# Kernel tuning notes

Measured on AMD Instinct MI355X. Metric: run time of the kernel, lower is better.

The kernel has to match this reference:

```python
import jax, jax.numpy as jnp
import numpy as np

EMBED = 1024
HEADS = 16
HEAD_DIM = EMBED // HEADS


def setup_inputs() -> dict:
    key = jax.random.key(0)
    ks = jax.random.split(key, 8)
    N, L = 2, 2048
    s = 0.02
    return {
        "values": jax.random.normal(ks[0], (N, L, EMBED), jnp.float32),
        "keys": jax.random.normal(ks[1], (N, L, EMBED), jnp.float32),
        "queries": jax.random.normal(ks[2], (N, L, EMBED), jnp.float32),
        # per-head projection weights, SHARED across heads (nn.Linear(head_dim, head_dim))
        "Wv": jax.random.normal(ks[3], (HEAD_DIM, HEAD_DIM), jnp.float32) * s,
        "Wk": jax.random.normal(ks[4], (HEAD_DIM, HEAD_DIM), jnp.float32) * s,
        "Wq": jax.random.normal(ks[5], (HEAD_DIM, HEAD_DIM), jnp.float32) * s,
        "Wo": jax.random.normal(ks[6], (EMBED, EMBED), jnp.float32) * s,
        "bo": jax.random.normal(ks[7], (EMBED,), jnp.float32) * s,
    }


def reference(values, keys, queries, Wv, Wk, Wq, Wo, bo):
    N, Lq, _ = queries.shape
    Lk = keys.shape[1]
    Lv = values.shape[1]
    # split heads: (N, L, H, D)
    v = values.reshape(N, Lv, HEADS, HEAD_DIM)
    k = keys.reshape(N, Lk, HEADS, HEAD_DIM)
    q = queries.reshape(N, Lq, HEADS, HEAD_DIM)
    # per-head linear (weight shared across heads); nn.Linear computes x @ W.T
    v = jnp.einsum('nlhd,ed->nlhe', v, Wv)
    k = jnp.einsum('nlhd,ed->nlhe', k, Wk)
    q = jnp.einsum('nlhd,ed->nlhe', q, Wq)
    # scores (N, H, Lq, Lk); NOTE: scale uses sqrt(embed_size), as in the original
    scores = jnp.einsum('nqhd,nkhd->nhqk', q, k) / jnp.sqrt(jnp.float32(EMBED))
    attn = jax.nn.softmax(scores, axis=-1)
    out = jnp.einsum('nhql,nlhd->nqhd', attn, v).reshape(N, Lq, EMBED)
    out = out @ Wo.T + bo
    return out
```

## Files before the change

### kernel.cpp

```cpp
#include <hip/hip_runtime.h>
#include <hip/hip_bf16.h>

#define EMBED 1024
#define HEADS 16
#define HD 64
#define NB 2
#define LSEQ 2048

typedef __bf16 bf16x8 __attribute__((ext_vector_type(8)));
typedef float f32x4 __attribute__((ext_vector_type(4)));

static __device__ __forceinline__ __bf16 f2b(float x) {
    union { __hip_bfloat16 h; __bf16 b; } u;
    u.h = __float2bfloat16(x);
    return u.b;
}
static __device__ __forceinline__ bf16x8 cvt8(float4 a, float4 b) {
    bf16x8 r;
    r[0] = f2b(a.x); r[1] = f2b(a.y); r[2] = f2b(a.z); r[3] = f2b(a.w);
    r[4] = f2b(b.x); r[5] = f2b(b.y); r[6] = f2b(b.z); r[7] = f2b(b.w);
    return r;
}
static __device__ __forceinline__ unsigned short b2u(float x) {
    union { __hip_bfloat16 h; unsigned short u; } c;
    c.h = __float2bfloat16(x);
    return c.u;
}

#define GLD16(g, l) __builtin_amdgcn_global_load_lds( \
    (const __attribute__((address_space(1))) void*)(g), \
    (__attribute__((address_space(3))) void*)(l), 16, 0, 0)


__global__ __launch_bounds__(256) void proj_kernel(
    const float* __restrict__ vals,
    const float* __restrict__ keys,
    const float* __restrict__ quer,
    const float* __restrict__ Wv,
    const float* __restrict__ Wk,
    const float* __restrict__ Wq,
    const float* __restrict__ Wo,
    __hip_bfloat16* __restrict__ QF,
    __hip_bfloat16* __restrict__ KF,
    __hip_bfloat16* __restrict__ VF,
    __hip_bfloat16* __restrict__ Wob)
{
    if (blockIdx.x >= 1536) {
        int base = ((blockIdx.x - 1536) * 256 + threadIdx.x) * 16;
#pragma unroll
        for (int j = 0; j < 16; j += 4) {
            float4 w4 = *(const float4*)(Wo + base + j);
            __hip_bfloat16 o[4] = {
                __float2bfloat16(w4.x), __float2bfloat16(w4.y),
                __float2bfloat16(w4.z), __float2bfloat16(w4.w)};
            *(ushort4*)(Wob + base + j) = *(const ushort4*)o;
        }
        return;
    }

    int b      = blockIdx.x;
    int tensor = b % 3;
    int rem    = b / 3;
    int n      = rem >> 8;
    int lt     = (rem >> 3) & 31;
    int hp     = rem & 7;
    int t = threadIdx.x, w = t >> 6, lane = t & 63;
    int m16 = lane & 15, quad = lane >> 4;
    int l0 = lt * 64 + w * 16;

    const float* X = (tensor == 0) ? quer : (tensor == 1 ? keys : vals);
    const float* W = (tensor == 0) ? Wq   : (tensor == 1 ? Wk   : Wv);
    float scale = (tensor == 0) ? (1.44269504088896340736f / 32.0f) : 1.0f;

    const float* xb = X + ((size_t)n * LSEQ + l0 + m16) * EMBED + (hp * 2) * HD + quad * 8;
    bf16x8 xf[2][2];
#pragma unroll
    for (int hh = 0; hh < 2; ++hh)
#pragma unroll
        for (int kk = 0; kk < 2; ++kk) {
            const float* xp = xb + hh * HD + kk * 32;
            xf[hh][kk] = cvt8(*(const float4*)xp, *(const float4*)(xp + 4));
        }

    bf16x8 wf[4][2];
#pragma unroll
    for (int f = 0; f < 4; ++f)
#pragma unroll
        for (int kk = 0; kk < 2; ++kk) {
            const float* wp = W + (f * 16 + m16) * HD + kk * 32 + quad * 8;
            wf[f][kk] = cvt8(*(const float4*)wp, *(const float4*)(wp + 4));
        }

#pragma unroll
    for (int hh = 0; hh < 2; ++hh) {
        int h = hp * 2 + hh;
        size_t nhb = (size_t)(n * HEADS + h) * 131072;
        if (tensor != 2) {
            f32x4 acc[4] = {};
#pragma unroll
            for (int f = 0; f < 4; ++f) {
                acc[f] = __builtin_amdgcn_mfma_f32_16x16x32_bf16(wf[f][0], xf[hh][0], acc[f], 0, 0, 0);
                acc[f] = __builtin_amdgcn_mfma_f32_16x16x32_bf16(wf[f][1], xf[hh][1], acc[f], 0, 0, 0);
            }
            int key = l0 + m16;
#pragma unroll
            for (int f = 0; f < 4; ++f) {
                union { ushort4 u; unsigned short s[4]; } p;
#pragma unroll
                for (int r = 0; r < 4; ++r) p.s[r] = b2u(acc[f][r] * scale);
                int kk   = f >> 1;
                int qk2  = (f & 1) * 2 + (quad >> 1);
                int j4   = (quad & 1) * 4;
                __hip_bfloat16* dst;
                if (tensor == 0) {
                    dst = QF + nhb + (size_t)(l0 >> 4) * 1024 + kk * 512
                        + (qk2 * 16 + m16) * 8 + j4;
                } else {
                    dst = KF + nhb + (size_t)(key >> 5) * 2048
                        + ((key & 1) * 2 + kk) * 512
                        + (qk2 * 16 + ((key & 31) >> 1)) * 8 + j4;
                }
                *(ushort4*)dst = p.u;
            }
        } else {
            f32x4 acc[4] = {};
#pragma unroll
            for (int f = 0; f < 4; ++f) {
                acc[f] = __builtin_amdgcn_mfma_f32_16x16x32_bf16(xf[hh][0], wf[f][0], acc[f], 0, 0, 0);
                acc[f] = __builtin_amdgcn_mfma_f32_16x16x32_bf16(xf[hh][1], wf[f][1], acc[f], 0, 0, 0);
            }
            int keyq  = l0 + quad * 4;
            int c     = keyq >> 5;
            int quadv = (keyq & 31) >> 3;
            int j4    = (quad & 1) * 4;
#pragma unroll
            for (int f = 0; f < 4; ++f) {
                union { ushort4 u; unsigned short s[4]; } p;
#pragma unroll
                for (int r = 0; r < 4; ++r) p.s[r] = b2u(acc[f][r]);
                __hip_bfloat16* dst = VF + nhb + (size_t)c * 2048 + f * 512
                    + quadv * 128 + m16 * 8 + j4;
                *(ushort4*)dst = p.u;
            }
        }
    }
}

#define CHUNKS 32

#define LOADK(KFR, c_) do { \
    const __hip_bfloat16* kc_ = kp + (size_t)(c_) * 2048; \
    KFR[0][0] = *(const bf16x8*)(kc_); \
    KFR[0][1] = *(const bf16x8*)(kc_ + 512); \
    KFR[1][0] = *(const bf16x8*)(kc_ + 1024); \
    KFR[1][1] = *(const bf16x8*)(kc_ + 1536); \
} while (0)

#define LOADV(c_) do { \
    const __hip_bfloat16* vc_ = vp + (size_t)(c_) * 2048; \
    vf[0] = *(const bf16x8*)(vc_); \
    vf[1] = *(const bf16x8*)(vc_ + 512); \
    vf[2] = *(const bf16x8*)(vc_ + 1024); \
    vf[3] = *(const bf16x8*)(vc_ + 1536); \
} while (0)

#define SCORE(KFR, BUF) do { \
    f32x4 s_[2][2]; \
    __builtin_amdgcn_s_setprio(1); \
    _Pragma("unroll") \
    for (int tq_ = 0; tq_ < 2; ++tq_) { \
        _Pragma("unroll") \
        for (int t2_ = 0; t2_ < 2; ++t2_) { \
            f32x4 z_; \
            z_ = __builtin_amdgcn_mfma_f32_16x16x32_bf16(qf[tq_][0], KFR[t2_][0], zf, 0, 0, 0); \
            z_ = __builtin_amdgcn_mfma_f32_16x16x32_bf16(qf[tq_][1], KFR[t2_][1], z_, 0, 0, 0); \
            s_[tq_][t2_] = z_; \
        } \
    } \
    __builtin_amdgcn_s_setprio(0); \
    _Pragma("unroll") \
    for (int tq_ = 0; tq_ < 2; ++tq_) { \
        _Pragma("unroll") \
        for (int r_ = 0; r_ < 4; ++r_) { \
            float e0_ = __builtin_amdgcn_exp2f(s_[tq_][0][r_]); \
            float e1_ = __builtin_amdgcn_exp2f(s_[tq_][1][r_]); \
            unsigned u_ = __builtin_amdgcn_perm( \
                __float_as_uint(e1_), __float_as_uint(e0_), 0x07060302); \
            *(unsigned*)&Pb[BUF][w][tq_ * 16 + quad * 4 + r_][2 * m16] = u_; \
        } \
    } \
} while (0)

#define PVSTEP(BUF) do { \
    bf16x8 pf0_ = *(const bf16x8*)&Pb[BUF][w][m16][quad * 8]; \
    bf16x8 pf1_ = *(const bf16x8*)&Pb[BUF][w][16 + m16][quad * 8]; \
    __builtin_amdgcn_s_setprio(1); \
    _Pragma("unroll") \
    for (int f_ = 0; f_ < 4; ++f_) { \
        of[0][f_] = __builtin_amdgcn_mfma_f32_16x16x32_bf16(pf0_, vf[f_], of[0][f_], 0, 0, 0); \
        of[1][f_] = __builtin_amdgcn_mfma_f32_16x16x32_bf16(pf1_, vf[f_], of[1][f_], 0, 0, 0); \
    } \
    lsa[0] = __builtin_amdgcn_mfma_f32_16x16x32_bf16(pf0_, onesf, lsa[0], 0, 0, 0); \
    lsa[1] = __builtin_amdgcn_mfma_f32_16x16x32_bf16(pf1_, onesf, lsa[1], 0, 0, 0); \
    __builtin_amdgcn_s_setprio(0); \
} while (0)

__global__ __launch_bounds__(256) void attn_kernel(
    const __hip_bfloat16* __restrict__ QF,
    const __hip_bfloat16* __restrict__ KF,
    const __hip_bfloat16* __restrict__ VF,
    __hip_bfloat16* __restrict__ AO,
    int nhbase)
{
    __shared__ __align__(16) __hip_bfloat16 Pb[2][4][32][40];

    int i  = blockIdx.x;
    int x  = i & 7, r2 = i >> 3;
    int nh = nhbase + x * 2 + (r2 >> 5);
    int qblk = r2 & 31;

    int t = threadIdx.x, w = t >> 6, lane = t & 63;
    int m16 = lane & 15, quad = lane >> 4;
    int qh = w & 1, kh = w >> 1;
    int q0 = qblk * 64 + qh * 32;
    size_t nhb = (size_t)nh * 131072;

    const __hip_bfloat16* qb = QF + nhb + (size_t)(q0 >> 4) * 1024 + lane * 8;
    bf16x8 qf[2][2];
#pragma unroll
    for (int tq = 0; tq < 2; ++tq)
#pragma unroll
        for (int kk = 0; kk < 2; ++kk)
            qf[tq][kk] = *(const bf16x8*)(qb + tq * 1024 + kk * 512);

    const __hip_bfloat16* kp = KF + nhb + (size_t)(kh * 32) * 2048 + lane * 8;
    const __hip_bfloat16* vp = VF + nhb + (size_t)(kh * 32) * 2048 + lane * 8;

    bf16x8 onesf;
#pragma unroll
    for (int j = 0; j < 8; ++j) onesf[j] = f2b(1.0f);
    const f32x4 zf = {};

    f32x4 of[2][4] = {};
    f32x4 lsa[2] = {};
    bf16x8 kfa[2][2], kfb[2][2], vf[4];

    LOADK(kfa, 0);
    LOADK(kfb, 1);
    SCORE(kfa, 0);
    LOADV(0);

#pragma unroll 1
    for (int tt = 0; tt < 15; ++tt) {
        int c = 2 * tt;
        LOADK(kfa, c + 2);
        SCORE(kfb, 1);
        PVSTEP(0);
        LOADV(c + 1);
        LOADK(kfb, c + 3);
        SCORE(kfa, 0);
        PVSTEP(1);
        LOADV(c + 2);
    }
    SCORE(kfb, 1);
    PVSTEP(0);
    LOADV(31);
    PVSTEP(1);

    __syncthreads();
    float* Cb = (float*)&Pb[0][0][0][0];
    if (kh == 1) {
        int base = qh * 2560;
#pragma unroll
        for (int tq = 0; tq < 2; ++tq)
#pragma unroll
            for (int f = 0; f < 4; ++f)
                *(f32x4*)&Cb[base + (tq * 4 + f) * 256 + lane * 4] = of[tq][f];
#pragma unroll
        for (int tq = 0; tq < 2; ++tq)
#pragma unroll
            for (int r = 0; r < 4; ++r)
                Cb[base + 2048 + (tq * 4 + r) * 64 + lane] = lsa[tq][r];
    }
    __syncthreads();
    if (kh == 0) {
        int base = qh * 2560;
#pragma unroll
        for (int tq = 0; tq < 2; ++tq)
#pragma unroll
            for (int f = 0; f < 4; ++f)
                of[tq][f] += *(const f32x4*)&Cb[base + (tq * 4 + f) * 256 + lane * 4];
        int n = nh >> 4, h = nh & 15;
#pragma unroll
        for (int tq = 0; tq < 2; ++tq)
#pragma unroll
            for (int r = 0; r < 4; ++r) {
                float lt2 = lsa[tq][r] + Cb[base + 2048 + (tq * 4 + r) * 64 + lane];
                float rinv = 1.0f / lt2;
                int qrow = q0 + tq * 16 + quad * 4 + r;
#pragma unroll
                for (int f = 0; f < 4; ++f) {
                    int col = h * HD + f * 16 + m16;
                    AO[((size_t)n * LSEQ + qrow) * EMBED + col] =
                        __float2bfloat16(of[tq][f][r] * rinv);
                }
            }
    }
}

__global__ __launch_bounds__(256) void outproj_kernel(
    const __hip_bfloat16* __restrict__ AO,
    const __hip_bfloat16* __restrict__ Wob,
    const float* __restrict__ bo,
    float* __restrict__ out)
{
    __shared__ __align__(16) __hip_bfloat16 As[2][2][64][32];
    __shared__ __align__(16) __hip_bfloat16 Bs[2][2][64][32];

    int b  = blockIdx.x;
    int wk = (b & 7) * 128 + (b >> 3);
    int mt = wk >> 4, nt = wk & 15;
    int m0 = mt * 64, n0 = nt * 64;
    int t = threadIdx.x, w = t >> 6, lane = t & 63;
    int m16 = lane & 15, quad = lane >> 4;

    int srow = lane >> 2;
    int scol = (lane & 3) * 8;

    const __hip_bfloat16* Ab = AO  + (size_t)m0 * EMBED;
    const __hip_bfloat16* Bb = Wob + (size_t)n0 * EMBED;

#define STAGE_OP(bb, k0_) do { \
    GLD16(Ab + (size_t)(w * 16 + srow) * EMBED + (k0_) +      scol, &As[bb][0][w * 16][0]); \
    GLD16(Ab + (size_t)(w * 16 + srow) * EMBED + (k0_) + 32 + scol, &As[bb][1][w * 16][0]); \
    GLD16(Bb + (size_t)(w * 16 + srow) * EMBED + (k0_) +      scol, &Bs[bb][0][w * 16][0]); \
    GLD16(Bb + (size_t)(w * 16 + srow) * EMBED + (k0_) + 32 + scol, &Bs[bb][1][w * 16][0]); \
} while (0)

    f32x4 acc[4] = {};
    STAGE_OP(0, 0);
    __syncthreads();

#pragma unroll 2
    for (int ks = 0; ks < 16; ++ks) {
        if (ks < 15) STAGE_OP((ks + 1) & 1, (ks + 1) * 64);
        int cur = ks & 1;
        bf16x8 af[2], bfr[2][4];
#pragma unroll
        for (int kk = 0; kk < 2; ++kk)
            af[kk] = *(const bf16x8*)&As[cur][kk][w * 16 + m16][quad * 8];
#pragma unroll
        for (int kk = 0; kk < 2; ++kk)
#pragma unroll
            for (int tb = 0; tb < 4; ++tb)
                bfr[kk][tb] = *(const bf16x8*)&Bs[cur][kk][tb * 16 + m16][quad * 8];
#pragma unroll
        for (int tb = 0; tb < 4; ++tb) {
            acc[tb] = __builtin_amdgcn_mfma_f32_16x16x32_bf16(af[0], bfr[0][tb], acc[tb], 0, 0, 0);
            acc[tb] = __builtin_amdgcn_mfma_f32_16x16x32_bf16(af[1], bfr[1][tb], acc[tb], 0, 0, 0);
        }
        __syncthreads();
    }

#pragma unroll
    for (int tb = 0; tb < 4; ++tb) {
        int col = n0 + tb * 16 + m16;
        float bias = bo[col];
#pragma unroll
        for (int r = 0; r < 4; ++r) {
            int row = m0 + w * 16 + quad * 4 + r;
            out[(size_t)row * EMBED + col] = acc[tb][r] + bias;
        }
    }
#undef STAGE_OP
}

extern "C" void kernel_launch(void* const* d_in, const int* in_sizes, int n_in,
                              void* d_out, int out_size, void* d_ws, size_t ws_size,
                              hipStream_t stream) {
    const float* vals = (const float*)d_in[0];
    const float* keys = (const float*)d_in[1];
    const float* quer = (const float*)d_in[2];
    const float* Wv   = (const float*)d_in[3];
    const float* Wk   = (const float*)d_in[4];
    const float* Wq   = (const float*)d_in[5];
    const float* Wo   = (const float*)d_in[6];
    const float* bo   = (const float*)d_in[7];
    float* out = (float*)d_out;

    __hip_bfloat16* ws = (__hip_bfloat16*)d_ws;
    const size_t PE = (size_t)NB * HEADS * LSEQ * HD;
    __hip_bfloat16* QF  = ws;
    __hip_bfloat16* KF  = ws + PE;
    __hip_bfloat16* VF  = ws + 2 * PE;
    __hip_bfloat16* AO  = ws + 3 * PE;
    __hip_bfloat16* Wob = ws + 4 * PE;

    proj_kernel<<<1536 + 256, 256, 0, stream>>>(
        vals, keys, quer, Wv, Wk, Wq, Wo, QF, KF, VF, Wob);
    attn_kernel<<<512, 256, 0, stream>>>(QF, KF, VF, AO, 0);
    attn_kernel<<<512, 256, 0, stream>>>(QF, KF, VF, AO, 16);
    outproj_kernel<<<1024, 256, 0, stream>>>(AO, Wob, bo, out);
}
```

Baseline: 171.6 us.

## Compute transposed scores so P stays in registers, merge attention launches

```diff
diff --git a/kernel.cpp b/kernel.cpp
--- a/kernel.cpp
+++ b/kernel.cpp
@@ -164,7 +164,7 @@
     vf[3] = *(const bf16x8*)(vc_ + 1536); \
 } while (0)
 
-#define SCORE(KFR, BUF) do { \
+#define SCOREX(KFR, PF) do { \
     f32x4 s_[2][2]; \
     __builtin_amdgcn_s_setprio(1); \
     _Pragma("unroll") \
@@ -172,8 +172,8 @@
         _Pragma("unroll") \
         for (int t2_ = 0; t2_ < 2; ++t2_) { \
             f32x4 z_; \
-            z_ = __builtin_amdgcn_mfma_f32_16x16x32_bf16(qf[tq_][0], KFR[t2_][0], zf, 0, 0, 0); \
-            z_ = __builtin_amdgcn_mfma_f32_16x16x32_bf16(qf[tq_][1], KFR[t2_][1], z_, 0, 0, 0); \
+            z_ = __builtin_amdgcn_mfma_f32_16x16x32_bf16(KFR[t2_][0], qf[tq_][0], zf, 0, 0, 0); \
+            z_ = __builtin_amdgcn_mfma_f32_16x16x32_bf16(KFR[t2_][1], qf[tq_][1], z_, 0, 0, 0); \
             s_[tq_][t2_] = z_; \
         } \
     } \
@@ -182,26 +182,21 @@
     for (int tq_ = 0; tq_ < 2; ++tq_) { \
         _Pragma("unroll") \
         for (int r_ = 0; r_ < 4; ++r_) { \
-            float e0_ = __builtin_amdgcn_exp2f(s_[tq_][0][r_]); \
-            float e1_ = __builtin_amdgcn_exp2f(s_[tq_][1][r_]); \
-            unsigned u_ = __builtin_amdgcn_perm( \
-                __float_as_uint(e1_), __float_as_uint(e0_), 0x07060302); \
-            *(unsigned*)&Pb[BUF][w][tq_ * 16 + quad * 4 + r_][2 * m16] = u_; \
+            PF[tq_][2 * r_]     = f2b(__builtin_amdgcn_exp2f(s_[tq_][0][r_])); \
+            PF[tq_][2 * r_ + 1] = f2b(__builtin_amdgcn_exp2f(s_[tq_][1][r_])); \
         } \
     } \
 } while (0)
 
-#define PVSTEP(BUF) do { \
-    bf16x8 pf0_ = *(const bf16x8*)&Pb[BUF][w][m16][quad * 8]; \
-    bf16x8 pf1_ = *(const bf16x8*)&Pb[BUF][w][16 + m16][quad * 8]; \
+#define PVX(PF) do { \
     __builtin_amdgcn_s_setprio(1); \
     _Pragma("unroll") \
     for (int f_ = 0; f_ < 4; ++f_) { \
-        of[0][f_] = __builtin_amdgcn_mfma_f32_16x16x32_bf16(pf0_, vf[f_], of[0][f_], 0, 0, 0); \
-        of[1][f_] = __builtin_amdgcn_mfma_f32_16x16x32_bf16(pf1_, vf[f_], of[1][f_], 0, 0, 0); \
+        of[0][f_] = __builtin_amdgcn_mfma_f32_16x16x32_bf16(vf[f_], PF[0], of[0][f_], 0, 0, 0); \
+        of[1][f_] = __builtin_amdgcn_mfma_f32_16x16x32_bf16(vf[f_], PF[1], of[1][f_], 0, 0, 0); \
     } \
-    lsa[0] = __builtin_amdgcn_mfma_f32_16x16x32_bf16(pf0_, onesf, lsa[0], 0, 0, 0); \
-    lsa[1] = __builtin_amdgcn_mfma_f32_16x16x32_bf16(pf1_, onesf, lsa[1], 0, 0, 0); \
+    lsa[0] = __builtin_amdgcn_mfma_f32_16x16x32_bf16(onesf, PF[0], lsa[0], 0, 0, 0); \
+    lsa[1] = __builtin_amdgcn_mfma_f32_16x16x32_bf16(onesf, PF[1], lsa[1], 0, 0, 0); \
     __builtin_amdgcn_s_setprio(0); \
 } while (0)
 
@@ -209,14 +204,13 @@
     const __hip_bfloat16* __restrict__ QF,
     const __hip_bfloat16* __restrict__ KF,
     const __hip_bfloat16* __restrict__ VF,
-    __hip_bfloat16* __restrict__ AO,
-    int nhbase)
+    __hip_bfloat16* __restrict__ AO)
 {
-    __shared__ __align__(16) __hip_bfloat16 Pb[2][4][32][40];
+    __shared__ __align__(16) float Cb[5120];
 
     int i  = blockIdx.x;
     int x  = i & 7, r2 = i >> 3;
-    int nh = nhbase + x * 2 + (r2 >> 5);
+    int nh = x * 4 + (r2 >> 5);
     int qblk = r2 & 31;
 
     int t = threadIdx.x, w = t >> 6, lane = t & 63;
@@ -243,32 +237,31 @@
 
     f32x4 of[2][4] = {};
     f32x4 lsa[2] = {};
-    bf16x8 kfa[2][2], kfb[2][2], vf[4];
-
-    LOADK(kfa, 0);
-    LOADK(kfb, 1);
-    SCORE(kfa, 0);
+    bf16x8 ka[2][2], kb[2][2], vf[4], pA[2], pB[2];
+
+    LOADK(ka, 0);
+    LOADK(kb, 1);
+    SCOREX(ka, pA);
     LOADV(0);
 
 #pragma unroll 1
     for (int tt = 0; tt < 15; ++tt) {
         int c = 2 * tt;
-        LOADK(kfa, c + 2);
-        SCORE(kfb, 1);
-        PVSTEP(0);
+        LOADK(ka, c + 2);
+        SCOREX(kb, pB);
+        PVX(pA);
         LOADV(c + 1);
-        LOADK(kfb, c + 3);
-        SCORE(kfa, 0);
-        PVSTEP(1);
+        LOADK(kb, c + 3);
+        SCOREX(ka, pA);
+        PVX(pB);
         LOADV(c + 2);
     }
-    SCORE(kfb, 1);
-    PVSTEP(0);
+    SCOREX(kb, pB);
+    PVX(pA);
     LOADV(31);
-    PVSTEP(1);
+    PVX(pB);
 
     __syncthreads();
-    float* Cb = (float*)&Pb[0][0][0][0];
     if (kh == 1) {
         int base = qh * 2560;
 #pragma unroll
@@ -278,9 +271,7 @@
                 *(f32x4*)&Cb[base + (tq * 4 + f) * 256 + lane * 4] = of[tq][f];
 #pragma unroll
         for (int tq = 0; tq < 2; ++tq)
-#pragma unroll
-            for (int r = 0; r < 4; ++r)
-                Cb[base + 2048 + (tq * 4 + r) * 64 + lane] = lsa[tq][r];
+            Cb[base + 2048 + tq * 64 + lane] = lsa[tq][0];
     }
     __syncthreads();
     if (kh == 0) {
@@ -292,19 +283,19 @@
                 of[tq][f] += *(const f32x4*)&Cb[base + (tq * 4 + f) * 256 + lane * 4];
         int n = nh >> 4, h = nh & 15;
 #pragma unroll
-        for (int tq = 0; tq < 2; ++tq)
-#pragma unroll
-            for (int r = 0; r < 4; ++r) {
-                float lt2 = lsa[tq][r] + Cb[base + 2048 + (tq * 4 + r) * 64 + lane];
-                float rinv = 1.0f / lt2;
-                int qrow = q0 + tq * 16 + quad * 4 + r;
-#pragma unroll
-                for (int f = 0; f < 4; ++f) {
-                    int col = h * HD + f * 16 + m16;
-                    AO[((size_t)n * LSEQ + qrow) * EMBED + col] =
-                        __float2bfloat16(of[tq][f][r] * rinv);
-                }
-            }
+        for (int tq = 0; tq < 2; ++tq) {
+            float lt2 = lsa[tq][0] + Cb[base + 2048 + tq * 64 + lane];
+            float rinv = 1.0f / lt2;
+            int qrow = q0 + tq * 16 + m16;
+#pragma unroll
+            for (int f = 0; f < 4; ++f) {
+                union { ushort4 u; unsigned short s[4]; } pk;
+#pragma unroll
+                for (int r = 0; r < 4; ++r) pk.s[r] = b2u(of[tq][f][r] * rinv);
+                int col = h * HD + f * 16 + quad * 4;
+                *(ushort4*)&AO[((size_t)n * LSEQ + qrow) * EMBED + col] = pk.u;
+            }
+        }
     }
 }
 
@@ -398,7 +389,6 @@
 
     proj_kernel<<<1536 + 256, 256, 0, stream>>>(
         vals, keys, quer, Wv, Wk, Wq, Wo, QF, KF, VF, Wob);
-    attn_kernel<<<512, 256, 0, stream>>>(QF, KF, VF, AO, 0);
-    attn_kernel<<<512, 256, 0, stream>>>(QF, KF, VF, AO, 16);
+    attn_kernel<<<1024, 256, 0, stream>>>(QF, KF, VF, AO);
     outproj_kernel<<<1024, 256, 0, stream>>>(AO, Wob, bo, out);
 }
```

After: 169.1 us. About the same (-1.5%).
